# Optimization experiments

Measured on AMD Instinct MI355X. Metric: run time of the kernel, lower is better.

Reference implementation:

```python
import jax, jax.numpy as jnp
import numpy as np

N_QUBITS = 6

def _apply_1q(state, U, w):
    # state: [B] + [2]*6 complex; U: [2,2] complex
    ax = 1 + w
    s = jnp.moveaxis(state, ax, -1)
    s = jnp.einsum('...j,ij->...i', s, U)
    return jnp.moveaxis(s, -1, ax)

def _apply_cnot(state, ctrl, tgt):
    ca, ta = 1 + ctrl, 1 + tgt
    s = jnp.moveaxis(state, (ca, ta), (1, 2))  # [B,2,2,...]
    s = jnp.stack([s[:, 0], s[:, 1, ::-1]], axis=1)
    return jnp.moveaxis(s, (1, 2), (ca, ta))

def _rot(phi, theta, omega):
    # PennyLane Rot = RZ(omega) RY(theta) RZ(phi)
    c, s = jnp.cos(theta / 2), jnp.sin(theta / 2)
    return jnp.stack([
        jnp.stack([jnp.exp(-0.5j * (phi + omega)) * c, -jnp.exp(0.5j * (phi - omega)) * s]),
        jnp.stack([jnp.exp(-0.5j * (phi - omega)) * s, jnp.exp(0.5j * (phi + omega)) * c]),
    ])

def _quantum(xq, qw):
    B = xq.shape[0]
    # AngleEmbedding RY: product state, per-qubit amplitudes [cos(x/2), sin(x/2)]
    amps = jnp.stack([jnp.cos(xq / 2), jnp.sin(xq / 2)], axis=-1)  # [B,6,2]
    state = amps[:, 0]
    for i in range(1, N_QUBITS):
        state = jnp.einsum('b...,bj->b...j', state, amps[:, i])
    state = state.astype(jnp.complex64)  # [B,2,2,2,2,2,2]
    # StronglyEntanglingLayers: per layer Rot on each wire, then CNOT ring of range r
    n_layers = qw.shape[0]
    for l in range(n_layers):
        for w in range(N_QUBITS):
            U = _rot(qw[l, w, 0], qw[l, w, 1], qw[l, w, 2])
            state = _apply_1q(state, U, w)
        r = (l % (N_QUBITS - 1)) + 1  # default ranges
        for w in range(N_QUBITS):
            state = _apply_cnot(state, w, (w + r) % N_QUBITS)
    probs = jnp.abs(state) ** 2
    zs = []
    for w in range(N_QUBITS):
        axes = tuple(a for a in range(1, N_QUBITS + 1) if a != 1 + w)
        p = jnp.sum(probs, axis=axes)  # [B,2]
        zs.append(p[:, 0] - p[:, 1])
    return jnp.stack(zs, axis=-1)  # [B,6]

def setup_inputs() -> dict:
    key = jax.random.key(0)
    ks = jax.random.split(key, 10)
    B = 16384
    return {
        'xc': jax.random.normal(ks[0], (B, 2048), jnp.float32),
        'xq': jax.random.uniform(ks[1], (B, N_QUBITS), jnp.float32),
        'W1': jax.random.normal(ks[2], (64, 2048), jnp.float32) * 0.02,
        'b1': jnp.zeros((64,), jnp.float32),
        'qw': jax.random.uniform(ks[3], (3, N_QUBITS, 3), jnp.float32, 0.0, 2 * np.pi),
        'Wq': jax.random.normal(ks[4], (16, N_QUBITS), jnp.float32) * 0.3,
        'bq': jnp.zeros((16,), jnp.float32),
        'Wf': jax.random.normal(ks[5], (3, 80), jnp.float32) * 0.1,
        'bf': jnp.zeros((3,), jnp.float32),
    }

def reference(xc, xq, W1, b1, qw, Wq, bq, Wf, bf):
    c = jax.nn.relu(xc @ W1.T + b1)                 # [B,64]
    q = _quantum(xq, qw) @ Wq.T + bq                # [B,16]
    return jnp.concatenate([c, q], axis=1) @ Wf.T + bf  # [B,3]
```

## Files before the change

kernel.cpp:

```cpp
#include <hip/hip_runtime.h>
#include <hip/hip_bf16.h>

#define NQ 6

typedef __attribute__((ext_vector_type(8))) short short8;
typedef __attribute__((ext_vector_type(4))) float floatx4;

#define WS_MQ_F   8192
#define WS_CQ_F   (8192+18)
#define WS_W1BF_B 36864
#define WS_QPART_B 301056

__global__ __launch_bounds__(64) void prep_kernel(
    const float* __restrict__ qw, int n_layers,
    const float* __restrict__ W1, const float* __restrict__ Wq,
    const float* __restrict__ bq, const float* __restrict__ Wf,
    const float* __restrict__ bf, float* __restrict__ ws_f,
    short* __restrict__ w1bf)
{
    const int blk  = blockIdx.x;
    const int lane = threadIdx.x;

    if (blk == 0) {
        if (lane < 18) {
            int j = lane / 6, wi = lane % 6;
            float s = 0.f;
            for (int m = 0; m < 16; ++m) s += Wf[j*80 + 64 + m] * Wq[m*6 + wi];
            ws_f[WS_MQ_F + lane] = s;
        } else if (lane < 21) {
            int j = lane - 18;
            float s = bf[j];
            for (int m = 0; m < 16; ++m) s += Wf[j*80 + 64 + m] * bq[m];
            ws_f[WS_CQ_F + j] = s;
        }
    } else if (blk <= 64) {
        const int j = blk - 1;
        float re = (lane == j) ? 1.f : 0.f;
        float im = 0.f;
        for (int l = 0; l < n_layers; ++l) {
            for (int w = 0; w < NQ; ++w) {
                const float* g = qw + (l*NQ + w)*3;
                float phi = g[0], th = g[1], om = g[2];
                float c, s;  __sincosf(0.5f*th, &s, &c);
                float sa, ca; __sincosf(0.5f*(phi+om), &sa, &ca);
                float sb, cb; __sincosf(0.5f*(phi-om), &sb, &cb);
                float u00r =  c*ca, u00i = -c*sa;
                float u01r = -s*cb, u01i = -s*sb;
                float u10r =  s*cb, u10i = -s*sb;
                float u11r =  c*ca, u11i =  c*sa;
                int p = 5 - w, mask = 1 << p;
                float pre = __shfl_xor(re, mask, 64);
                float pim = __shfl_xor(im, mask, 64);
                int b = (lane >> p) & 1;
                float mr = b ? u11r : u00r, mi = b ? u11i : u00i;
                float pr = b ? u10r : u01r, pi = b ? u10i : u01i;
                float nre = mr*re - mi*im + pr*pre - pi*pim;
                float nim = mr*im + mi*re + pr*pim + pi*pre;
                re = nre; im = nim;
            }
            int r = l % (NQ-1) + 1;
            for (int w = 0; w < NQ; ++w) {
                int tgt = (w + r) % NQ;
                int tmask = 1 << (5 - tgt);
                float pre = __shfl_xor(re, tmask, 64);
                float pim = __shfl_xor(im, tmask, 64);
                int cs = (lane >> (5 - w)) & 1;
                re = cs ? pre : re;
                im = cs ? pim : im;
            }
        }
        ws_f[(lane*64 + j)*2 + 0] = re;
        ws_f[(lane*64 + j)*2 + 1] = im;
    } else {
        int idx = (blk - 65)*512 + lane*8;
        if (idx < 64*2048) {
            float4 a0 = *(const float4*)(W1 + idx);
            float4 a1 = *(const float4*)(W1 + idx + 4);
            union { short8 v; __hip_bfloat162 h[4]; } u;
            float2 f;
            f.x=a0.x; f.y=a0.y; u.h[0] = __float22bfloat162_rn(f);
            f.x=a0.z; f.y=a0.w; u.h[1] = __float22bfloat162_rn(f);
            f.x=a1.x; f.y=a1.y; u.h[2] = __float22bfloat162_rn(f);
            f.x=a1.z; f.y=a1.w; u.h[3] = __float22bfloat162_rn(f);
            *(short8*)(w1bf + idx) = u.v;
        }
    }
}

__global__ __launch_bounds__(256) void qpart_kernel(
    const float* __restrict__ xq, const float2* __restrict__ U,
    const float* __restrict__ ws_f, float* __restrict__ qpart, int B)
{
    const int lane = threadIdx.x & 63;
    const int t = __builtin_amdgcn_readfirstlane((int)(threadIdx.x >> 6));
    const int b = blockIdx.x*64 + lane;

    float a[64];
    const float* x = xq + (size_t)b*6;
    a[0] = 1.f;
    #pragma unroll
    for (int q = 0; q < 6; ++q) {
        float c, s; __sincosf(0.5f*x[q], &s, &c);
        const int sz = 1 << q;
        #pragma unroll
        for (int m = sz-1; m >= 0; --m) {
            float v = a[m];
            a[2*m+1] = v*s;
            a[2*m+0] = v*c;
        }
    }

    float zp[6] = {0,0,0,0,0,0};
    const float2* Urow = U + t*16*64;
    for (int ii = 0; ii < 16; ++ii) {
        float rr = 0.f, ri = 0.f;
        #pragma unroll
        for (int j = 0; j < 64; ++j) {
            float2 u = Urow[ii*64 + j];
            rr += u.x * a[j];
            ri += u.y * a[j];
        }
        float p = rr*rr + ri*ri;
        int i = t*16 + ii;
        #pragma unroll
        for (int w = 0; w < 6; ++w) zp[w] += ((i >> (5-w)) & 1) ? -p : p;
    }

    __shared__ float zbuf[4][64][6];
    #pragma unroll
    for (int w = 0; w < 6; ++w) zbuf[t][lane][w] = zp[w];
    __syncthreads();
    if (t == 0) {
        float z[6];
        #pragma unroll
        for (int w = 0; w < 6; ++w)
            z[w] = zbuf[0][lane][w] + zbuf[1][lane][w] + zbuf[2][lane][w] + zbuf[3][lane][w];
        #pragma unroll
        for (int j = 0; j < 3; ++j) {
            float v = ws_f[WS_CQ_F + j];
            #pragma unroll
            for (int w = 0; w < 6; ++w) v += ws_f[WS_MQ_F + j*6 + w] * z[w];
            qpart[(size_t)b*3 + j] = v;
        }
    }
}

__global__ __launch_bounds__(128) void gemm_kernel(
    const float* __restrict__ xc, const short* __restrict__ w1bf,
    const float* __restrict__ b1, const float* __restrict__ Wf,
    const float* __restrict__ qpart, float* __restrict__ out, int B)
{
    const int tid = threadIdx.x;
    const int wv  = tid >> 6;
    const int l   = tid & 63;
    const int blk = blockIdx.x;

    const int row  = blk*32 + wv*16 + (l & 15);
    const int koff = (l >> 4) * 8;

    const float* ap = xc + (size_t)row*2048 + koff;
    const short* bp = w1bf + (l & 15)*2048 + koff;

    floatx4 acc0 = {0,0,0,0}, acc1 = {0,0,0,0}, acc2 = {0,0,0,0}, acc3 = {0,0,0,0};

    #pragma unroll 4
    for (int kk = 0; kk < 64; ++kk) {
        float4 a0 = *(const float4*)ap;
        float4 a1 = *(const float4*)(ap + 4);
        union { short8 v; __hip_bfloat162 h[4]; } af;
        float2 f;
        f.x=a0.x; f.y=a0.y; af.h[0] = __float22bfloat162_rn(f);
        f.x=a0.z; f.y=a0.w; af.h[1] = __float22bfloat162_rn(f);
        f.x=a1.x; f.y=a1.y; af.h[2] = __float22bfloat162_rn(f);
        f.x=a1.z; f.y=a1.w; af.h[3] = __float22bfloat162_rn(f);

        short8 b0 = *(const short8*)(bp);
        short8 bv1 = *(const short8*)(bp + 16*2048);
        short8 b2 = *(const short8*)(bp + 32*2048);
        short8 b3 = *(const short8*)(bp + 48*2048);

        acc0 = __builtin_amdgcn_mfma_f32_16x16x32_bf16(af.v, b0,  acc0, 0, 0, 0);
        acc1 = __builtin_amdgcn_mfma_f32_16x16x32_bf16(af.v, bv1, acc1, 0, 0, 0);
        acc2 = __builtin_amdgcn_mfma_f32_16x16x32_bf16(af.v, b2,  acc2, 0, 0, 0);
        acc3 = __builtin_amdgcn_mfma_f32_16x16x32_bf16(af.v, b3,  acc3, 0, 0, 0);

        ap += 32;
        bp += 32;
    }

    __shared__ float cl[32][65];
    const int rbase = wv*16 + (l >> 4)*4;
    const int c0 = l & 15;
    float bb0 = b1[c0], bb1 = b1[16 + c0], bb2 = b1[32 + c0], bb3 = b1[48 + c0];
    #pragma unroll
    for (int r = 0; r < 4; ++r) {
        cl[rbase + r][ 0 + c0] = fmaxf(acc0[r] + bb0, 0.f);
        cl[rbase + r][16 + c0] = fmaxf(acc1[r] + bb1, 0.f);
        cl[rbase + r][32 + c0] = fmaxf(acc2[r] + bb2, 0.f);
        cl[rbase + r][48 + c0] = fmaxf(acc3[r] + bb3, 0.f);
    }
    __syncthreads();

    const int rr = tid & 31;
    const int j  = tid >> 5;
    if (j < 3) {
        float v = 0.f;
        #pragma unroll
        for (int col = 0; col < 64; ++col) v += Wf[j*80 + col] * cl[rr][col];
        int g = blk*32 + rr;
        out[(size_t)g*3 + j] = v + qpart[(size_t)g*3 + j];
    }
}

extern "C" void kernel_launch(void* const* d_in, const int* in_sizes, int n_in,
                              void* d_out, int out_size, void* d_ws, size_t ws_size,
                              hipStream_t stream) {
    const float* xc = (const float*)d_in[0];
    const float* xq = (const float*)d_in[1];
    const float* W1 = (const float*)d_in[2];
    const float* b1 = (const float*)d_in[3];
    const float* qw = (const float*)d_in[4];
    const float* Wq = (const float*)d_in[5];
    const float* bq = (const float*)d_in[6];
    const float* Wf = (const float*)d_in[7];
    const float* bf = (const float*)d_in[8];
    float* out = (float*)d_out;

    const int B = in_sizes[1] / NQ;
    const int n_layers = in_sizes[4] / (NQ * 3);

    char* ws = (char*)d_ws;
    float*  ws_f  = (float*)ws;
    float2* U     = (float2*)ws;
    short*  w1bf  = (short*)(ws + WS_W1BF_B);
    float*  qpart = (float*)(ws + WS_QPART_B);

    prep_kernel<<<dim3(321), dim3(64), 0, stream>>>(qw, n_layers, W1, Wq, bq, Wf, bf, ws_f, w1bf);
    qpart_kernel<<<dim3(B/64), dim3(256), 0, stream>>>(xq, U, ws_f, qpart, B);
    gemm_kernel<<<dim3(B/32), dim3(128), 0, stream>>>(xc, w1bf, b1, Wf, qpart, out, B);
}
```

Before: 239.5 us.

## Fuse quantum-part and GEMM kernels, add register prefetch in K loop

Merges the quantum expectation kernel and the bf16 MFMA GEMM into one kernel with 64-row blocks of 256 threads. The quantum result stays in shared memory instead of going through a global qpart buffer, which also removes one launch. The K loop now loads the next iteration's A and B fragments into registers before the current MFMAs, to hide global load latency. The fused kernel needs more registers (the 64-float amplitude array plus prefetch buffers), which may lower occupancy, and the GEMM now runs serially after the quantum phase inside each block.

```diff
diff --git a/kernel.cpp b/kernel.cpp
--- a/kernel.cpp
+++ b/kernel.cpp
@@ -9,7 +9,6 @@
 #define WS_MQ_F   8192
 #define WS_CQ_F   (8192+18)
 #define WS_W1BF_B 36864
-#define WS_QPART_B 301056
 
 __global__ __launch_bounds__(64) void prep_kernel(
     const float* __restrict__ qw, int n_layers,
@@ -87,48 +86,57 @@
     }
 }
 
-__global__ __launch_bounds__(256) void qpart_kernel(
+__global__ __launch_bounds__(256) void fused_kernel(
     const float* __restrict__ xq, const float2* __restrict__ U,
-    const float* __restrict__ ws_f, float* __restrict__ qpart, int B)
+    const float* __restrict__ ws_f,
+    const float* __restrict__ xc, const short* __restrict__ w1bf,
+    const float* __restrict__ b1, const float* __restrict__ Wf,
+    float* __restrict__ out)
 {
-    const int lane = threadIdx.x & 63;
-    const int t = __builtin_amdgcn_readfirstlane((int)(threadIdx.x >> 6));
-    const int b = blockIdx.x*64 + lane;
-
-    float a[64];
-    const float* x = xq + (size_t)b*6;
-    a[0] = 1.f;
-    #pragma unroll
-    for (int q = 0; q < 6; ++q) {
-        float c, s; __sincosf(0.5f*x[q], &s, &c);
-        const int sz = 1 << q;
-        #pragma unroll
-        for (int m = sz-1; m >= 0; --m) {
-            float v = a[m];
-            a[2*m+1] = v*s;
-            a[2*m+0] = v*c;
-        }
-    }
-
-    float zp[6] = {0,0,0,0,0,0};
-    const float2* Urow = U + t*16*64;
-    for (int ii = 0; ii < 16; ++ii) {
-        float rr = 0.f, ri = 0.f;
-        #pragma unroll
-        for (int j = 0; j < 64; ++j) {
-            float2 u = Urow[ii*64 + j];
-            rr += u.x * a[j];
-            ri += u.y * a[j];
-        }
-        float p = rr*rr + ri*ri;
-        int i = t*16 + ii;
-        #pragma unroll
-        for (int w = 0; w < 6; ++w) zp[w] += ((i >> (5-w)) & 1) ? -p : p;
-    }
+    const int tid  = threadIdx.x;
+    const int lane = tid & 63;
+    const int t    = __builtin_amdgcn_readfirstlane((int)(tid >> 6));
+    const int blk  = blockIdx.x;
 
     __shared__ float zbuf[4][64][6];
-    #pragma unroll
-    for (int w = 0; w < 6; ++w) zbuf[t][lane][w] = zp[w];
+    __shared__ float qres[64][3];
+    __shared__ float cl[64][65];
+
+    {
+        const int b = blk*64 + lane;
+        float a[64];
+        const float* x = xq + (size_t)b*6;
+        a[0] = 1.f;
+        #pragma unroll
+        for (int q = 0; q < 6; ++q) {
+            float c, s; __sincosf(0.5f*x[q], &s, &c);
+            const int sz = 1 << q;
+            #pragma unroll
+            for (int m = sz-1; m >= 0; --m) {
+                float v = a[m];
+                a[2*m+1] = v*s;
+                a[2*m+0] = v*c;
+            }
+        }
+
+        float zp[6] = {0,0,0,0,0,0};
+        const float2* Urow = U + t*16*64;
+        for (int ii = 0; ii < 16; ++ii) {
+            float rr = 0.f, ri = 0.f;
+            #pragma unroll
+            for (int j = 0; j < 64; ++j) {
+                float2 u = Urow[ii*64 + j];
+                rr += u.x * a[j];
+                ri += u.y * a[j];
+            }
+            float p = rr*rr + ri*ri;
+            int i = t*16 + ii;
+            #pragma unroll
+            for (int w = 0; w < 6; ++w) zp[w] += ((i >> (5-w)) & 1) ? -p : p;
+        }
+        #pragma unroll
+        for (int w = 0; w < 6; ++w) zbuf[t][lane][w] = zp[w];
+    }
     __syncthreads();
     if (t == 0) {
         float z[6];
@@ -140,33 +148,36 @@
             float v = ws_f[WS_CQ_F + j];
             #pragma unroll
             for (int w = 0; w < 6; ++w) v += ws_f[WS_MQ_F + j*6 + w] * z[w];
-            qpart[(size_t)b*3 + j] = v;
-        }
-    }
-}
-
-__global__ __launch_bounds__(128) void gemm_kernel(
-    const float* __restrict__ xc, const short* __restrict__ w1bf,
-    const float* __restrict__ b1, const float* __restrict__ Wf,
-    const float* __restrict__ qpart, float* __restrict__ out, int B)
-{
-    const int tid = threadIdx.x;
-    const int wv  = tid >> 6;
-    const int l   = tid & 63;
-    const int blk = blockIdx.x;
-
-    const int row  = blk*32 + wv*16 + (l & 15);
-    const int koff = (l >> 4) * 8;
+            qres[lane][j] = v;
+        }
+    }
+
+    const int row  = blk*64 + t*16 + (lane & 15);
+    const int koff = (lane >> 4) * 8;
 
     const float* ap = xc + (size_t)row*2048 + koff;
-    const short* bp = w1bf + (l & 15)*2048 + koff;
+    const short* bp = w1bf + (lane & 15)*2048 + koff;
 
     floatx4 acc0 = {0,0,0,0}, acc1 = {0,0,0,0}, acc2 = {0,0,0,0}, acc3 = {0,0,0,0};
 
+    float4 a0  = *(const float4*)ap;
+    float4 a1  = *(const float4*)(ap + 4);
+    short8 b0  = *(const short8*)(bp);
+    short8 bv1 = *(const short8*)(bp + 16*2048);
+    short8 b2  = *(const short8*)(bp + 32*2048);
+    short8 b3  = *(const short8*)(bp + 48*2048);
+
     #pragma unroll 4
-    for (int kk = 0; kk < 64; ++kk) {
-        float4 a0 = *(const float4*)ap;
-        float4 a1 = *(const float4*)(ap + 4);
+    for (int kk = 1; kk < 64; ++kk) {
+        const float* apn = ap + kk*32;
+        const short* bpn = bp + kk*32;
+        float4 na0 = *(const float4*)apn;
+        float4 na1 = *(const float4*)(apn + 4);
+        short8 nb0 = *(const short8*)(bpn);
+        short8 nb1 = *(const short8*)(bpn + 16*2048);
+        short8 nb2 = *(const short8*)(bpn + 32*2048);
+        short8 nb3 = *(const short8*)(bpn + 48*2048);
+
         union { short8 v; __hip_bfloat162 h[4]; } af;
         float2 f;
         f.x=a0.x; f.y=a0.y; af.h[0] = __float22bfloat162_rn(f);
@@ -174,23 +185,28 @@
         f.x=a1.x; f.y=a1.y; af.h[2] = __float22bfloat162_rn(f);
         f.x=a1.z; f.y=a1.w; af.h[3] = __float22bfloat162_rn(f);
 
-        short8 b0 = *(const short8*)(bp);
-        short8 bv1 = *(const short8*)(bp + 16*2048);
-        short8 b2 = *(const short8*)(bp + 32*2048);
-        short8 b3 = *(const short8*)(bp + 48*2048);
-
         acc0 = __builtin_amdgcn_mfma_f32_16x16x32_bf16(af.v, b0,  acc0, 0, 0, 0);
         acc1 = __builtin_amdgcn_mfma_f32_16x16x32_bf16(af.v, bv1, acc1, 0, 0, 0);
         acc2 = __builtin_amdgcn_mfma_f32_16x16x32_bf16(af.v, b2,  acc2, 0, 0, 0);
         acc3 = __builtin_amdgcn_mfma_f32_16x16x32_bf16(af.v, b3,  acc3, 0, 0, 0);
 
-        ap += 32;
-        bp += 32;
-    }
-
-    __shared__ float cl[32][65];
-    const int rbase = wv*16 + (l >> 4)*4;
-    const int c0 = l & 15;
+        a0 = na0; a1 = na1; b0 = nb0; bv1 = nb1; b2 = nb2; b3 = nb3;
+    }
+    {
+        union { short8 v; __hip_bfloat162 h[4]; } af;
+        float2 f;
+        f.x=a0.x; f.y=a0.y; af.h[0] = __float22bfloat162_rn(f);
+        f.x=a0.z; f.y=a0.w; af.h[1] = __float22bfloat162_rn(f);
+        f.x=a1.x; f.y=a1.y; af.h[2] = __float22bfloat162_rn(f);
+        f.x=a1.z; f.y=a1.w; af.h[3] = __float22bfloat162_rn(f);
+        acc0 = __builtin_amdgcn_mfma_f32_16x16x32_bf16(af.v, b0,  acc0, 0, 0, 0);
+        acc1 = __builtin_amdgcn_mfma_f32_16x16x32_bf16(af.v, bv1, acc1, 0, 0, 0);
+        acc2 = __builtin_amdgcn_mfma_f32_16x16x32_bf16(af.v, b2,  acc2, 0, 0, 0);
+        acc3 = __builtin_amdgcn_mfma_f32_16x16x32_bf16(af.v, b3,  acc3, 0, 0, 0);
+    }
+
+    const int rbase = t*16 + ((lane >> 4) * 4);
+    const int c0 = lane & 15;
     float bb0 = b1[c0], bb1 = b1[16 + c0], bb2 = b1[32 + c0], bb3 = b1[48 + c0];
     #pragma unroll
     for (int r = 0; r < 4; ++r) {
@@ -201,14 +217,13 @@
     }
     __syncthreads();
 
-    const int rr = tid & 31;
-    const int j  = tid >> 5;
-    if (j < 3) {
+    const int rr2 = tid & 63;
+    if (t < 3) {
         float v = 0.f;
         #pragma unroll
-        for (int col = 0; col < 64; ++col) v += Wf[j*80 + col] * cl[rr][col];
-        int g = blk*32 + rr;
-        out[(size_t)g*3 + j] = v + qpart[(size_t)g*3 + j];
+        for (int col = 0; col < 64; ++col) v += Wf[t*80 + col] * cl[rr2][col];
+        int g = blk*64 + rr2;
+        out[(size_t)g*3 + t] = v + qres[rr2][t];
     }
 }
 
@@ -233,9 +248,7 @@
     float*  ws_f  = (float*)ws;
     float2* U     = (float2*)ws;
     short*  w1bf  = (short*)(ws + WS_W1BF_B);
-    float*  qpart = (float*)(ws + WS_QPART_B);
 
     prep_kernel<<<dim3(321), dim3(64), 0, stream>>>(qw, n_layers, W1, Wq, bq, Wf, bf, ws_f, w1bf);
-    qpart_kernel<<<dim3(B/64), dim3(256), 0, stream>>>(xq, U, ws_f, qpart, B);
-    gemm_kernel<<<dim3(B/32), dim3(128), 0, stream>>>(xc, w1bf, b1, Wf, qpart, out, B);
+    fused_kernel<<<dim3(B/64), dim3(256), 0, stream>>>(xq, U, ws_f, xc, w1bf, b1, Wf, out);
 }
```

Result: slower. 245.2 us (+2.4%).
